# Performance work log

Measured on AMD Instinct MI355X. Metric: run time of the kernel, lower is better.

Reference implementation:

```python
import jax, jax.numpy as jnp
import numpy as np

D_MODEL = 1024
N_HEADS = 16
BATCH = 2
SEQ = 2048


def get_freqs(seq, n_dim):
    # standard RoPE frequencies: [seq, n_dim//2]
    inv_freq = 1.0 / (10000.0 ** (jnp.arange(0, n_dim, 2, dtype=jnp.float32) / n_dim))
    return jnp.arange(seq, dtype=jnp.float32)[:, None] * inv_freq[None, :]


def rope(x, freqs):
    # x: [batch, seq, heads, n_dim]; half-split rotation convention
    half = x.shape[-1] // 2
    cos = jnp.cos(freqs)[None, :, None, :]  # [1, seq, 1, half]
    sin = jnp.sin(freqs)[None, :, None, :]
    x1, x2 = x[..., :half], x[..., half:]
    return jnp.concatenate([x1 * cos - x2 * sin, x1 * sin + x2 * cos], axis=-1)


def setup_inputs() -> dict:
    key = jax.random.key(0)
    ks = jax.random.split(key, 5)
    x = jax.random.normal(ks[0], (BATCH, SEQ, D_MODEL), dtype=jnp.float32)
    qw = jax.random.normal(ks[1], (D_MODEL, D_MODEL), dtype=jnp.float32)
    kw = jax.random.normal(ks[2], (D_MODEL, D_MODEL), dtype=jnp.float32)
    vw = jax.random.normal(ks[3], (D_MODEL, D_MODEL), dtype=jnp.float32)
    ow = jax.random.normal(ks[4], (D_MODEL, D_MODEL), dtype=jnp.float32)
    return {"x": x, "qw": qw, "kw": kw, "vw": vw, "ow": ow}


def reference(x, qw, kw, vw, ow):
    batch, seq, dim = x.shape
    n_heads = N_HEADS
    n_dim = dim // n_heads
    Q = (x @ qw).reshape(batch, seq, n_heads, n_dim)
    K = (x @ kw).reshape(batch, seq, n_heads, n_dim)
    V = (x @ vw).reshape(batch, seq, n_heads, n_dim)
    freqs = get_freqs(seq, n_dim)
    Q = rope(Q, freqs)
    K = rope(K, freqs)
    # NOTE: original divides by sqrt(d_model), not sqrt(head_dim)
    scale = 1.0 / jnp.sqrt(jnp.float32(dim))
    score = jnp.einsum('bqhd,bkhd->bhqk', Q, K) * scale
    weights = jax.nn.softmax(score.astype(jnp.float32), axis=-1)
    attn = jnp.einsum('bhqk,bkhd->bqhd', weights, V)
    merged = attn.reshape(batch, seq, dim)
    return merged @ ow
```

## Files before the change

kernel.cpp:

```cpp
#include <hip/hip_runtime.h>
#include <math.h>

#define DM 1024
#define NH 16
#define HD 64
#define BB 2
#define SS 2048
#define MM (BB*SS)

typedef unsigned short ushort_t;
typedef __attribute__((ext_vector_type(8))) short short8;
typedef __attribute__((ext_vector_type(4))) short short4_t;
typedef __attribute__((ext_vector_type(4))) float floatx4;

__device__ __forceinline__ ushort_t f2bf(float f) {
    return (ushort_t)((__float_as_uint(f) + 0x8000u) >> 16);
}
__device__ __forceinline__ float bf2f(ushort_t h) {
    return __uint_as_float(((unsigned int)h) << 16);
}

__device__ __forceinline__ void gl_lds16(const ushort_t* g, ushort_t* l) {
    __builtin_amdgcn_global_load_lds(
        (const __attribute__((address_space(1))) unsigned int*)g,
        (__attribute__((address_space(3))) unsigned int*)l, 16, 0, 0);
}

__global__ __launch_bounds__(256) void freq_kernel(float2* __restrict__ ct)
{
    const int idx = blockIdx.x * 256 + threadIdx.x;
    const int s = idx >> 5, j = idx & 31;
    const float invf = powf(10000.f, -(float)j * (1.f / 32.f));
    float sn, cs;
    sincosf((float)s * invf, &sn, &cs);
    ct[idx] = make_float2(cs, sn);
}

__global__ __launch_bounds__(256) void convert_x(const float* __restrict__ X,
                                                 ushort_t* __restrict__ Xh,
                                                 ushort_t* __restrict__ Xl)
{
    const size_t base = ((size_t)blockIdx.x * 256 + threadIdx.x) * 8;
    float v[8];
    *(float4*)&v[0] = *(const float4*)(X + base);
    *(float4*)&v[4] = *(const float4*)(X + base + 4);
    short8 h, l;
#pragma unroll
    for (int i = 0; i < 8; ++i) {
        const ushort_t hi = f2bf(v[i]);
        h[i] = (short)hi;
        l[i] = (short)f2bf(v[i] - bf2f(hi));
    }
    *(short8*)(Xh + base) = h;
    *(short8*)(Xl + base) = l;
}

__global__ __launch_bounds__(256) void convert_w4(
    const float* __restrict__ qw, const float* __restrict__ kw,
    const float* __restrict__ vw, const float* __restrict__ ow,
    ushort_t* __restrict__ qkh, ushort_t* __restrict__ qkl,
    ushort_t* __restrict__ vwt, ushort_t* __restrict__ owt)
{
    const int which = blockIdx.z;
    const float* W;
    ushort_t *Th, *Tl = nullptr;
    bool split = which < 2;
    if (which == 0)      { W = qw; Th = qkh; Tl = qkl; }
    else if (which == 1) { W = kw; Th = qkh + (size_t)DM * DM; Tl = qkl + (size_t)DM * DM; }
    else if (which == 2) { W = vw; Th = vwt; }
    else                 { W = ow; Th = owt; }

    __shared__ float tile[64][65];
    const int t  = threadIdx.x;
    const int kb = blockIdx.y * 64, nb = blockIdx.x * 64;
    const int r  = t >> 2;
    const int c0 = (t & 3) * 16;
#pragma unroll
    for (int i = 0; i < 4; ++i)
        *(float4*)&tile[r][c0 + 4 * i] = *(const float4*)(W + (size_t)(kb + r) * DM + nb + c0 + 4 * i);
    __syncthreads();
    ushort_t hi[16], lo[16];
#pragma unroll
    for (int i = 0; i < 16; ++i) {
        const float v = tile[c0 + i][r];
        hi[i] = f2bf(v);
        lo[i] = f2bf(v - bf2f(hi[i]));
    }
    const size_t dst = (size_t)(nb + r) * DM + kb + c0;
    *(short8*)(Th + dst)     = *(short8*)&hi[0];
    *(short8*)(Th + dst + 8) = *(short8*)&hi[8];
    if (split) {
        *(short8*)(Tl + dst)     = *(short8*)&lo[0];
        *(short8*)(Tl + dst + 8) = *(short8*)&lo[8];
    }
}

#define GTM 128

template<int UPR, int SH>
__device__ __forceinline__ void stage_tile(const ushort_t* __restrict__ G,
                                           ushort_t* L, int rows, int w, int lane)
{
    const int iters = rows * UPR / 256;
#pragma unroll
    for (int i = 0; i < iters; ++i) {
        const int p0 = (i * 4 + w) * 64;
        const int p  = p0 + lane;
        const int r  = p / UPR;
        const int u  = (p % UPR) ^ ((r >> SH) & (UPR - 1));
        gl_lds16(G + (size_t)r * DM + u * 8, L + (size_t)p0 * 8);
    }
}

template<int UPR, int SH>
__device__ __forceinline__ short8 frag(const ushort_t* L, int r, int u)
{
    const int uu = u ^ ((r >> SH) & (UPR - 1));
    return *(const short8*)&L[((size_t)r * UPR + uu) * 8];
}

template<int SPLIT, int OUT_MODE, int TN, int BK>
__global__ __launch_bounds__(256, 2) void gemm_mfma(
    const ushort_t* __restrict__ Ah, const ushort_t* __restrict__ Al,
    const ushort_t* __restrict__ Bh, const ushort_t* __restrict__ Bl,
    float* __restrict__ Cf, ushort_t* __restrict__ Cb, ushort_t* __restrict__ Cb2,
    const float2* __restrict__ CT)
{
    constexpr int UPR = BK / 8;
    constexpr int KC  = BK / 32;
    constexpr int NI  = TN / 32;
    constexpr int SH  = (UPR == 4) ? 1 : 0;
    constexpr int NSTEP = DM / BK;

    __shared__ __align__(16) ushort_t AsH[2][GTM * BK];
    __shared__ __align__(16) ushort_t BsH[2][TN * BK];
    __shared__ __align__(16) ushort_t AsL[2][SPLIT ? GTM * BK : 8];
    __shared__ __align__(16) ushort_t BsL[2][SPLIT ? TN * BK : 8];
    __shared__ __align__(16) ushort_t Ts[(OUT_MODE == 2) ? 64 * 136 : 8];

    const int t    = threadIdx.x;
    const int w    = t >> 6;
    const int lane = t & 63;
    const int col  = lane & 15;
    const int quad = lane >> 4;
    const int wm   = w & 1;
    const int wn   = w >> 1;
    const int m0   = blockIdx.y * GTM;
    const int n0   = blockIdx.x * TN;

    const ushort_t* Abase = Ah + (size_t)m0 * DM;
    const ushort_t* Bbase = Bh + (size_t)n0 * DM;
    const ushort_t* AbaseL = SPLIT ? Al + (size_t)m0 * DM : nullptr;
    const ushort_t* BbaseL = SPLIT ? Bl + (size_t)n0 * DM : nullptr;

    floatx4 acc[4][NI];
#pragma unroll
    for (int mi = 0; mi < 4; ++mi)
#pragma unroll
        for (int ni = 0; ni < NI; ++ni) acc[mi][ni] = (floatx4){0.f, 0.f, 0.f, 0.f};

    stage_tile<UPR, SH>(Abase, AsH[0], GTM, w, lane);
    if (SPLIT) stage_tile<UPR, SH>(AbaseL, AsL[0], GTM, w, lane);
    stage_tile<UPR, SH>(Bbase, BsH[0], TN, w, lane);
    if (SPLIT) stage_tile<UPR, SH>(BbaseL, BsL[0], TN, w, lane);

    for (int ks = 0; ks < NSTEP; ++ks) {
        const int cur = ks & 1;
        __syncthreads();
        if (ks + 1 < NSTEP) {
            const int k1 = (ks + 1) * BK;
            stage_tile<UPR, SH>(Abase + k1, AsH[cur ^ 1], GTM, w, lane);
            if (SPLIT) stage_tile<UPR, SH>(AbaseL + k1, AsL[cur ^ 1], GTM, w, lane);
            stage_tile<UPR, SH>(Bbase + k1, BsH[cur ^ 1], TN, w, lane);
            if (SPLIT) stage_tile<UPR, SH>(BbaseL + k1, BsL[cur ^ 1], TN, w, lane);
        }

#pragma unroll
        for (int kc = 0; kc < KC; ++kc) {
            short8 ah[4], bh[NI];
            short8 al[SPLIT ? 4 : 1], bl[SPLIT ? NI : 1];
#pragma unroll
            for (int mi = 0; mi < 4; ++mi) {
                const int r = wm * 64 + mi * 16 + col;
                ah[mi] = frag<UPR, SH>(AsH[cur], r, kc * 4 + quad);
                if (SPLIT) al[mi] = frag<UPR, SH>(AsL[cur], r, kc * 4 + quad);
            }
#pragma unroll
            for (int ni = 0; ni < NI; ++ni) {
                const int r = wn * (TN / 2) + ni * 16 + col;
                bh[ni] = frag<UPR, SH>(BsH[cur], r, kc * 4 + quad);
                if (SPLIT) bl[ni] = frag<UPR, SH>(BsL[cur], r, kc * 4 + quad);
            }
#pragma unroll
            for (int mi = 0; mi < 4; ++mi)
#pragma unroll
                for (int ni = 0; ni < NI; ++ni) {
                    acc[mi][ni] = __builtin_amdgcn_mfma_f32_16x16x32_bf16(ah[mi], bh[ni], acc[mi][ni], 0, 0, 0);
                    if (SPLIT) {
                        acc[mi][ni] = __builtin_amdgcn_mfma_f32_16x16x32_bf16(al[mi], bh[ni], acc[mi][ni], 0, 0, 0);
                        acc[mi][ni] = __builtin_amdgcn_mfma_f32_16x16x32_bf16(ah[mi], bl[ni], acc[mi][ni], 0, 0, 0);
                    }
                }
        }
    }

    if constexpr (OUT_MODE == 0) {
#pragma unroll
        for (int mi = 0; mi < 4; ++mi)
#pragma unroll
            for (int ni = 0; ni < NI; ++ni)
#pragma unroll
                for (int r = 0; r < 4; ++r) {
                    const int m = m0 + wm * 64 + mi * 16 + quad * 4 + r;
                    const int n = n0 + wn * (TN / 2) + ni * 16 + col;
                    Cf[(size_t)m * DM + n] = acc[mi][ni][r];
                }
    }
    if constexpr (OUT_MODE == 2) {
#pragma unroll
        for (int mi = 0; mi < 4; ++mi)
#pragma unroll
            for (int ni = 0; ni < NI; ++ni) {
                const int nl = wn * (TN / 2) + ni * 16 + col;
                const int ml = wm * 64 + mi * 16 + quad * 4;
                short4_t pk;
#pragma unroll
                for (int r = 0; r < 4; ++r) pk[r] = (short)f2bf(acc[mi][ni][r]);
                *(short4_t*)&Ts[nl * 136 + ml] = pk;
            }
        __syncthreads();
        const int b = m0 >> 11, h = n0 >> 6;
        const int s0 = m0 & (SS - 1);
#pragma unroll
        for (int it = 0; it < 4; ++it) {
            const int idx = it * 256 + t;
            const int dr = idx >> 4, u = idx & 15;
            const short8 v = *(const short8*)&Ts[dr * 136 + u * 8];
            *(short8*)(Cb + ((size_t)((b << 4) + h) * HD + dr) * SS + s0 + u * 8) = v;
        }
    }
    if constexpr (OUT_MODE == 3) {
        const int tn = n0 >> 10;
#pragma unroll
        for (int mi = 0; mi < 4; ++mi)
#pragma unroll
            for (int ni = 0; ni < 2; ++ni)
#pragma unroll
                for (int r = 0; r < 4; ++r) {
                    const int m = m0 + wm * 64 + mi * 16 + quad * 4 + r;
                    const int n = n0 + wn * (TN / 2) + ni * 16 + col;
                    const int b = m >> 11, s = m & (SS - 1);
                    const int h = (n >> 6) & 15, d = n & 63;
                    const float2 cs = CT[(s << 5) + d];
                    const float x1 = acc[mi][ni][r];
                    const float x2 = acc[mi][ni + 2][r];
                    const float y1 = x1 * cs.x - x2 * cs.y;
                    const float y2 = x1 * cs.y + x2 * cs.x;
                    const size_t base = ((size_t)((b << 4) + h) * SS + s) * HD + d;
                    if (tn == 0) {
                        Cf[base]      = y1 * (1.f / 32.f);
                        Cf[base + 32] = y2 * (1.f / 32.f);
                    } else {
                        const ushort_t h1 = f2bf(y1), h2 = f2bf(y2);
                        Cb [base]      = h1;
                        Cb [base + 32] = h2;
                        Cb2[base]      = f2bf(y1 - bf2f(h1));
                        Cb2[base + 32] = f2bf(y2 - bf2f(h2));
                    }
                }
    }
}

__device__ __forceinline__ short8 afrag(const ushort_t* S, int r, int lu)
{
    return *(const short8*)&S[(size_t)(((r << 3) | (lu ^ (r & 7))) << 3)];
}

__device__ __forceinline__ void attn_stage(const ushort_t* __restrict__ KhB,
                                           const ushort_t* __restrict__ KlB,
                                           const ushort_t* __restrict__ VtB,
                                           int k0, ushort_t* dKh, ushort_t* dKl,
                                           ushort_t* dVt, int w, int lane)
{
#pragma unroll
    for (int i = 0; i < 4; ++i) {
        const int p0 = (i * 2 + w) * 64;
        const int p  = p0 + lane;
        const int r  = p >> 3;
        const int gu = (p & 7) ^ (r & 7);
        gl_lds16(KhB + (size_t)(k0 + r) * HD + gu * 8, dKh + (size_t)p0 * 8);
        gl_lds16(KlB + (size_t)(k0 + r) * HD + gu * 8, dKl + (size_t)p0 * 8);
        gl_lds16(VtB + (size_t)r * SS + k0 + gu * 8,   dVt + (size_t)p0 * 8);
    }
}

__global__ __launch_bounds__(128, 1) void attn_mfma3(
    const float* __restrict__ Qh, const ushort_t* __restrict__ Khi,
    const ushort_t* __restrict__ Klo, const ushort_t* __restrict__ Vt,
    ushort_t* __restrict__ Mgb)
{
    __shared__ __align__(16) ushort_t KhiS[2][64 * 64];
    __shared__ __align__(16) ushort_t KloS[2][64 * 64];
    __shared__ __align__(16) ushort_t VtS [2][64 * 64];
    __shared__ __align__(16) ushort_t PS  [128 * 64];

    const int t    = threadIdx.x;
    const int w    = t >> 6;
    const int lane = t & 63;
    const int col  = lane & 15;
    const int quad = lane >> 4;

    const int bh = blockIdx.y;
    const int q0 = blockIdx.x * 128;
    const float*    Qb  = Qh  + (size_t)bh * SS * HD;
    const ushort_t* KhB = Khi + (size_t)bh * SS * HD;
    const ushort_t* KlB = Klo + (size_t)bh * SS * HD;
    const ushort_t* VtB = Vt  + (size_t)bh * HD * SS;

    short8 qhi[4][2], qlo[4][2];
#pragma unroll
    for (int mi = 0; mi < 4; ++mi) {
#pragma unroll
        for (int ch = 0; ch < 2; ++ch) {
            const float* p = Qb + (size_t)(q0 + w * 64 + mi * 16 + col) * HD + ch * 32 + quad * 8;
            const float4 a = *(const float4*)p;
            const float4 b = *(const float4*)(p + 4);
            float v[8] = {a.x, a.y, a.z, a.w, b.x, b.y, b.z, b.w};
#pragma unroll
            for (int j = 0; j < 8; ++j) {
                const ushort_t h = f2bf(v[j]);
                qhi[mi][ch][j] = (short)h;
                qlo[mi][ch][j] = (short)f2bf(v[j] - bf2f(h));
            }
        }
    }

    floatx4 Oacc[4][4];
#pragma unroll
    for (int mi = 0; mi < 4; ++mi)
#pragma unroll
        for (int nt = 0; nt < 4; ++nt) Oacc[mi][nt] = (floatx4){0.f, 0.f, 0.f, 0.f};
    float mstat[4] = {-1e30f, -1e30f, -1e30f, -1e30f};
    float lstat[4] = {0.f, 0.f, 0.f, 0.f};

    attn_stage(KhB, KlB, VtB, 0, KhiS[0], KloS[0], VtS[0], w, lane);

    for (int kt0 = 0; kt0 < SS / 64; ++kt0) {
        const int cur = kt0 & 1;
        __syncthreads();
        if (kt0 + 1 < SS / 64)
            attn_stage(KhB, KlB, VtB, (kt0 + 1) * 64,
                       KhiS[cur ^ 1], KloS[cur ^ 1], VtS[cur ^ 1], w, lane);

        floatx4 sc[4][4];
#pragma unroll
        for (int kt = 0; kt < 4; ++kt) {
            short8 kh[2], kl[2];
#pragma unroll
            for (int ch = 0; ch < 2; ++ch) {
                kh[ch] = afrag(KhiS[cur], kt * 16 + col, ch * 4 + quad);
                kl[ch] = afrag(KloS[cur], kt * 16 + col, ch * 4 + quad);
            }
#pragma unroll
            for (int mi = 0; mi < 4; ++mi) {
                floatx4 a = (floatx4){0.f, 0.f, 0.f, 0.f};
#pragma unroll
                for (int ch = 0; ch < 2; ++ch)
                    a = __builtin_amdgcn_mfma_f32_16x16x32_bf16(kh[ch], qhi[mi][ch], a, 0, 0, 0);
#pragma unroll
                for (int ch = 0; ch < 2; ++ch)
                    a = __builtin_amdgcn_mfma_f32_16x16x32_bf16(kh[ch], qlo[mi][ch], a, 0, 0, 0);
#pragma unroll
                for (int ch = 0; ch < 2; ++ch)
                    a = __builtin_amdgcn_mfma_f32_16x16x32_bf16(kl[ch], qhi[mi][ch], a, 0, 0, 0);
                sc[kt][mi] = a;
            }
        }

#pragma unroll
        for (int mi = 0; mi < 4; ++mi) {
            float mloc = -1e30f;
#pragma unroll
            for (int kt = 0; kt < 4; ++kt)
#pragma unroll
                for (int r = 0; r < 4; ++r) mloc = fmaxf(mloc, sc[kt][mi][r]);
            mloc = fmaxf(mloc, __shfl_xor(mloc, 16));
            mloc = fmaxf(mloc, __shfl_xor(mloc, 32));
            const float mnew  = fmaxf(mstat[mi], mloc);
            const float alpha = __expf(mstat[mi] - mnew);
            mstat[mi] = mnew;

            float psum = 0.f;
            const int qrow = w * 64 + mi * 16 + col;
#pragma unroll
            for (int kt = 0; kt < 4; ++kt) {
                short4_t pk;
#pragma unroll
                for (int r = 0; r < 4; ++r) {
                    const float p = __expf(sc[kt][mi][r] - mnew);
                    psum += p;
                    pk[r] = (short)f2bf(p);
                }
                const int u = (kt * 2 + (quad >> 1)) ^ (col & 7);
                *(short4_t*)&PS[(qrow << 6) + (u << 3) + ((quad & 1) << 2)] = pk;
            }
            psum += __shfl_xor(psum, 16);
            psum += __shfl_xor(psum, 32);
            lstat[mi] = lstat[mi] * alpha + psum;

            floatx4 alr;
#pragma unroll
            for (int r = 0; r < 4; ++r) alr[r] = __shfl(alpha, quad * 4 + r, 64);
#pragma unroll
            for (int nt = 0; nt < 4; ++nt)
#pragma unroll
                for (int r = 0; r < 4; ++r) Oacc[mi][nt][r] *= alr[r];
        }

        short8 pf[4][2];
#pragma unroll
        for (int mi = 0; mi < 4; ++mi)
#pragma unroll
            for (int ch = 0; ch < 2; ++ch)
                pf[mi][ch] = afrag(PS, w * 64 + mi * 16 + col, ch * 4 + quad);
#pragma unroll
        for (int nt = 0; nt < 4; ++nt) {
            short8 vf[2];
#pragma unroll
            for (int ch = 0; ch < 2; ++ch)
                vf[ch] = afrag(VtS[cur], nt * 16 + col, ch * 4 + quad);
#pragma unroll
            for (int mi = 0; mi < 4; ++mi)
#pragma unroll
                for (int ch = 0; ch < 2; ++ch)
                    Oacc[mi][nt] = __builtin_amdgcn_mfma_f32_16x16x32_bf16(pf[mi][ch], vf[ch], Oacc[mi][nt], 0, 0, 0);
        }
    }

    const int b = bh >> 4, h = bh & 15;
#pragma unroll
    for (int mi = 0; mi < 4; ++mi) {
        floatx4 linv;
#pragma unroll
        for (int r = 0; r < 4; ++r) linv[r] = 1.f / __shfl(lstat[mi], quad * 4 + r, 64);
#pragma unroll
        for (int nt = 0; nt < 4; ++nt)
#pragma unroll
            for (int r = 0; r < 4; ++r) {
                const int srow = q0 + w * 64 + mi * 16 + quad * 4 + r;
                Mgb[(size_t)(b * SS + srow) * DM + h * HD + nt * 16 + col] =
                    f2bf(Oacc[mi][nt][r] * linv[r]);
            }
    }
}

extern "C" void kernel_launch(void* const* d_in, const int* in_sizes, int n_in,
                              void* d_out, int out_size, void* d_ws, size_t ws_size,
                              hipStream_t stream)
{
    const float* x  = (const float*)d_in[0];
    const float* qw = (const float*)d_in[1];
    const float* kw = (const float*)d_in[2];
    const float* vw = (const float*)d_in[3];
    const float* ow = (const float*)d_in[4];
    float* out = (float*)d_out;

    float*    Qh  = (float*)d_ws;
    ushort_t* Khi = (ushort_t*)(Qh + (size_t)MM * DM);
    ushort_t* Klo = Khi + (size_t)MM * DM;
    ushort_t* Vtb = Klo + (size_t)MM * DM;
    ushort_t* Mgb = Vtb + (size_t)MM * DM;
    ushort_t* xh  = Mgb + (size_t)MM * DM;
    ushort_t* xl  = xh  + (size_t)MM * DM;
    ushort_t* qkh = xl  + (size_t)MM * DM;
    ushort_t* qkl = qkh + (size_t)2048 * DM;
    ushort_t* vwt = qkl + (size_t)2048 * DM;
    ushort_t* owt = vwt + (size_t)DM * DM;
    float2*   ct  = (float2*)(owt + (size_t)DM * DM);

    freq_kernel<<<(SS * 32) / 256, 256, 0, stream>>>(ct);
    convert_x<<<(MM * DM) / (256 * 8), 256, 0, stream>>>(x, xh, xl);
    convert_w4<<<dim3(16, 16, 4), 256, 0, stream>>>(qw, kw, vw, ow, qkh, qkl, vwt, owt);

    gemm_mfma<1, 3, 128, 32><<<dim3(2048 / 128, MM / GTM), 256, 0, stream>>>(
        xh, xl, qkh, qkl, Qh, Khi, Klo, ct);
    gemm_mfma<0, 2, 64, 64><<<dim3(DM / 64, MM / GTM), 256, 0, stream>>>(
        xh, nullptr, vwt, nullptr, nullptr, Vtb, nullptr, nullptr);

    attn_mfma3<<<dim3(SS / 128, BB * NH), 128, 0, stream>>>(Qh, Khi, Klo, Vtb, Mgb);

    gemm_mfma<0, 0, 64, 64><<<dim3(DM / 64, MM / GTM), 256, 0, stream>>>(
        Mgb, nullptr, owt, nullptr, out, nullptr, nullptr, nullptr);
}
```

Before: 306.9 us.

## Split attention over key halves with 256-thread blocks and a combine pass

Attention now splits the key range into two halves across a new grid z dimension, doubling the block count. Each block uses 256 threads with 32 query rows per wave, which reduces per-thread register state. Each half writes its unnormalized output and per-row max and sum, and a separate combine kernel rescales and merges them. The double-buffered async K/V staging is replaced by a single buffer with two barriers per tile, which gives up load/compute overlap. It also adds an extra kernel and a round trip of the partial outputs through global memory, reusing the xh/xl workspace.

```diff
diff --git a/kernel.cpp b/kernel.cpp
--- a/kernel.cpp
+++ b/kernel.cpp
@@ -276,32 +276,15 @@
     return *(const short8*)&S[(size_t)(((r << 3) | (lu ^ (r & 7))) << 3)];
 }
 
-__device__ __forceinline__ void attn_stage(const ushort_t* __restrict__ KhB,
-                                           const ushort_t* __restrict__ KlB,
-                                           const ushort_t* __restrict__ VtB,
-                                           int k0, ushort_t* dKh, ushort_t* dKl,
-                                           ushort_t* dVt, int w, int lane)
-{
-#pragma unroll
-    for (int i = 0; i < 4; ++i) {
-        const int p0 = (i * 2 + w) * 64;
-        const int p  = p0 + lane;
-        const int r  = p >> 3;
-        const int gu = (p & 7) ^ (r & 7);
-        gl_lds16(KhB + (size_t)(k0 + r) * HD + gu * 8, dKh + (size_t)p0 * 8);
-        gl_lds16(KlB + (size_t)(k0 + r) * HD + gu * 8, dKl + (size_t)p0 * 8);
-        gl_lds16(VtB + (size_t)r * SS + k0 + gu * 8,   dVt + (size_t)p0 * 8);
-    }
-}
-
-__global__ __launch_bounds__(128, 1) void attn_mfma3(
+__global__ __launch_bounds__(256, 2) void attn_split(
     const float* __restrict__ Qh, const ushort_t* __restrict__ Khi,
     const ushort_t* __restrict__ Klo, const ushort_t* __restrict__ Vt,
-    ushort_t* __restrict__ Mgb)
-{
-    __shared__ __align__(16) ushort_t KhiS[2][64 * 64];
-    __shared__ __align__(16) ushort_t KloS[2][64 * 64];
-    __shared__ __align__(16) ushort_t VtS [2][64 * 64];
+    ushort_t* __restrict__ Op0, ushort_t* __restrict__ Op1,
+    float2* __restrict__ ML)
+{
+    __shared__ __align__(16) ushort_t KhiS[64 * 64];
+    __shared__ __align__(16) ushort_t KloS[64 * 64];
+    __shared__ __align__(16) ushort_t VtS [64 * 64];
     __shared__ __align__(16) ushort_t PS  [128 * 64];
 
     const int t    = threadIdx.x;
@@ -310,19 +293,21 @@
     const int col  = lane & 15;
     const int quad = lane >> 4;
 
-    const int bh = blockIdx.y;
-    const int q0 = blockIdx.x * 128;
+    const int bh   = blockIdx.y;
+    const int q0   = blockIdx.x * 128;
+    const int z    = blockIdx.z;
+    const int koff = z * (SS / 2);
     const float*    Qb  = Qh  + (size_t)bh * SS * HD;
     const ushort_t* KhB = Khi + (size_t)bh * SS * HD;
     const ushort_t* KlB = Klo + (size_t)bh * SS * HD;
     const ushort_t* VtB = Vt  + (size_t)bh * HD * SS;
 
-    short8 qhi[4][2], qlo[4][2];
-#pragma unroll
-    for (int mi = 0; mi < 4; ++mi) {
+    short8 qhi[2][2], qlo[2][2];
+#pragma unroll
+    for (int mi = 0; mi < 2; ++mi) {
 #pragma unroll
         for (int ch = 0; ch < 2; ++ch) {
-            const float* p = Qb + (size_t)(q0 + w * 64 + mi * 16 + col) * HD + ch * 32 + quad * 8;
+            const float* p = Qb + (size_t)(q0 + w * 32 + mi * 16 + col) * HD + ch * 32 + quad * 8;
             const float4 a = *(const float4*)p;
             const float4 b = *(const float4*)(p + 4);
             float v[8] = {a.x, a.y, a.z, a.w, b.x, b.y, b.z, b.w};
@@ -335,34 +320,39 @@
         }
     }
 
-    floatx4 Oacc[4][4];
-#pragma unroll
-    for (int mi = 0; mi < 4; ++mi)
+    floatx4 Oacc[2][4];
+#pragma unroll
+    for (int mi = 0; mi < 2; ++mi)
 #pragma unroll
         for (int nt = 0; nt < 4; ++nt) Oacc[mi][nt] = (floatx4){0.f, 0.f, 0.f, 0.f};
-    float mstat[4] = {-1e30f, -1e30f, -1e30f, -1e30f};
-    float lstat[4] = {0.f, 0.f, 0.f, 0.f};
-
-    attn_stage(KhB, KlB, VtB, 0, KhiS[0], KloS[0], VtS[0], w, lane);
-
-    for (int kt0 = 0; kt0 < SS / 64; ++kt0) {
-        const int cur = kt0 & 1;
+    float mstat[2] = {-1e30f, -1e30f}, lstat[2] = {0.f, 0.f};
+
+    for (int kt0 = 0; kt0 < (SS / 2) / 64; ++kt0) {
+        const int k0 = koff + kt0 * 64;
         __syncthreads();
-        if (kt0 + 1 < SS / 64)
-            attn_stage(KhB, KlB, VtB, (kt0 + 1) * 64,
-                       KhiS[cur ^ 1], KloS[cur ^ 1], VtS[cur ^ 1], w, lane);
-
-        floatx4 sc[4][4];
+#pragma unroll
+        for (int i = 0; i < 2; ++i) {
+            const int p0 = w * 128 + i * 64;
+            const int p  = p0 + lane;
+            const int r  = p >> 3;
+            const int gu = (p & 7) ^ (r & 7);
+            gl_lds16(KhB + (size_t)(k0 + r) * HD + gu * 8, KhiS + (size_t)p0 * 8);
+            gl_lds16(KlB + (size_t)(k0 + r) * HD + gu * 8, KloS + (size_t)p0 * 8);
+            gl_lds16(VtB + (size_t)r * SS + k0 + gu * 8,   VtS  + (size_t)p0 * 8);
+        }
+        __syncthreads();
+
+        floatx4 sc[4][2];
 #pragma unroll
         for (int kt = 0; kt < 4; ++kt) {
             short8 kh[2], kl[2];
 #pragma unroll
             for (int ch = 0; ch < 2; ++ch) {
-                kh[ch] = afrag(KhiS[cur], kt * 16 + col, ch * 4 + quad);
-                kl[ch] = afrag(KloS[cur], kt * 16 + col, ch * 4 + quad);
-            }
-#pragma unroll
-            for (int mi = 0; mi < 4; ++mi) {
+                kh[ch] = afrag(KhiS, kt * 16 + col, ch * 4 + quad);
+                kl[ch] = afrag(KloS, kt * 16 + col, ch * 4 + quad);
+            }
+#pragma unroll
+            for (int mi = 0; mi < 2; ++mi) {
                 floatx4 a = (floatx4){0.f, 0.f, 0.f, 0.f};
 #pragma unroll
                 for (int ch = 0; ch < 2; ++ch)
@@ -378,7 +368,7 @@
         }
 
 #pragma unroll
-        for (int mi = 0; mi < 4; ++mi) {
+        for (int mi = 0; mi < 2; ++mi) {
             float mloc = -1e30f;
 #pragma unroll
             for (int kt = 0; kt < 4; ++kt)
@@ -391,7 +381,7 @@
             mstat[mi] = mnew;
 
             float psum = 0.f;
-            const int qrow = w * 64 + mi * 16 + col;
+            const int qrow = w * 32 + mi * 16 + col;
 #pragma unroll
             for (int kt = 0; kt < 4; ++kt) {
                 short4_t pk;
@@ -417,41 +407,70 @@
                 for (int r = 0; r < 4; ++r) Oacc[mi][nt][r] *= alr[r];
         }
 
-        short8 pf[4][2];
-#pragma unroll
-        for (int mi = 0; mi < 4; ++mi)
+        short8 pf[2][2];
+#pragma unroll
+        for (int mi = 0; mi < 2; ++mi)
 #pragma unroll
             for (int ch = 0; ch < 2; ++ch)
-                pf[mi][ch] = afrag(PS, w * 64 + mi * 16 + col, ch * 4 + quad);
+                pf[mi][ch] = afrag(PS, w * 32 + mi * 16 + col, ch * 4 + quad);
 #pragma unroll
         for (int nt = 0; nt < 4; ++nt) {
             short8 vf[2];
 #pragma unroll
             for (int ch = 0; ch < 2; ++ch)
-                vf[ch] = afrag(VtS[cur], nt * 16 + col, ch * 4 + quad);
-#pragma unroll
-            for (int mi = 0; mi < 4; ++mi)
+                vf[ch] = afrag(VtS, nt * 16 + col, ch * 4 + quad);
+#pragma unroll
+            for (int mi = 0; mi < 2; ++mi)
 #pragma unroll
                 for (int ch = 0; ch < 2; ++ch)
                     Oacc[mi][nt] = __builtin_amdgcn_mfma_f32_16x16x32_bf16(pf[mi][ch], vf[ch], Oacc[mi][nt], 0, 0, 0);
         }
     }
 
+    ushort_t* dst = z ? Op1 : Op0;
     const int b = bh >> 4, h = bh & 15;
 #pragma unroll
-    for (int mi = 0; mi < 4; ++mi) {
-        floatx4 linv;
-#pragma unroll
-        for (int r = 0; r < 4; ++r) linv[r] = 1.f / __shfl(lstat[mi], quad * 4 + r, 64);
+    for (int mi = 0; mi < 2; ++mi) {
 #pragma unroll
         for (int nt = 0; nt < 4; ++nt)
 #pragma unroll
             for (int r = 0; r < 4; ++r) {
-                const int srow = q0 + w * 64 + mi * 16 + quad * 4 + r;
-                Mgb[(size_t)(b * SS + srow) * DM + h * HD + nt * 16 + col] =
-                    f2bf(Oacc[mi][nt][r] * linv[r]);
-            }
-    }
+                const int srow = q0 + w * 32 + mi * 16 + quad * 4 + r;
+                dst[(size_t)(b * SS + srow) * DM + h * HD + nt * 16 + col] =
+                    f2bf(Oacc[mi][nt][r]);
+            }
+        if (quad == 0) {
+            const int srow = q0 + w * 32 + mi * 16 + col;
+            ML[((size_t)z * 32 + bh) * SS + srow] = make_float2(mstat[mi], lstat[mi]);
+        }
+    }
+}
+
+__global__ __launch_bounds__(256) void attn_combine(
+    ushort_t* __restrict__ Op0, const ushort_t* __restrict__ Op1,
+    const float2* __restrict__ ML)
+{
+    const size_t idx8 = ((size_t)blockIdx.x * 256 + threadIdx.x) * 8;
+    const int row  = (int)(idx8 >> 10);
+    const int hcol = (int)(idx8 & 1023);
+    const int h = hcol >> 6;
+    const int b = row >> 11, s = row & (SS - 1);
+    const int bh = (b << 4) + h;
+
+    const float2 ml0 = ML[(size_t)bh * SS + s];
+    const float2 ml1 = ML[((size_t)32 + bh) * SS + s];
+    const float m  = fmaxf(ml0.x, ml1.x);
+    const float s0 = __expf(ml0.x - m);
+    const float s1 = __expf(ml1.x - m);
+    const float inv = 1.f / (s0 * ml0.y + s1 * ml1.y);
+
+    const short8 a = *(const short8*)(Op0 + idx8);
+    const short8 c = *(const short8*)(Op1 + idx8);
+    short8 o;
+#pragma unroll
+    for (int i = 0; i < 8; ++i)
+        o[i] = (short)f2bf((s0 * bf2f((ushort_t)a[i]) + s1 * bf2f((ushort_t)c[i])) * inv);
+    *(short8*)(Op0 + idx8) = o;
 }
 
 extern "C" void kernel_launch(void* const* d_in, const int* in_sizes, int n_in,
@@ -478,6 +497,9 @@
     ushort_t* owt = vwt + (size_t)DM * DM;
     float2*   ct  = (float2*)(owt + (size_t)DM * DM);
 
+    ushort_t* Op1 = xh;
+    float2*   ML  = (float2*)xl;
+
     freq_kernel<<<(SS * 32) / 256, 256, 0, stream>>>(ct);
     convert_x<<<(MM * DM) / (256 * 8), 256, 0, stream>>>(x, xh, xl);
     convert_w4<<<dim3(16, 16, 4), 256, 0, stream>>>(qw, kw, vw, ow, qkh, qkl, vwt, owt);
@@ -487,7 +509,9 @@
     gemm_mfma<0, 2, 64, 64><<<dim3(DM / 64, MM / GTM), 256, 0, stream>>>(
         xh, nullptr, vwt, nullptr, nullptr, Vtb, nullptr, nullptr);
 
-    attn_mfma3<<<dim3(SS / 128, BB * NH), 128, 0, stream>>>(Qh, Khi, Klo, Vtb, Mgb);
+    attn_split<<<dim3(SS / 128, BB * NH, 2), 256, 0, stream>>>(
+        Qh, Khi, Klo, Vtb, Mgb, Op1, ML);
+    attn_combine<<<(MM * DM) / (256 * 8), 256, 0, stream>>>(Mgb, Op1, ML);
 
     gemm_mfma<0, 0, 64, 64><<<dim3(DM / 64, MM / GTM), 256, 0, stream>>>(
         Mgb, nullptr, owt, nullptr, out, nullptr, nullptr, nullptr);
```

Measured after the change: 279.0 us. 9.1% less time.
